# Performance work log

Measured on AMD Instinct MI355X. Metric: run time of the kernel, lower is better.

Reference implementation:

```python
import jax, jax.numpy as jnp
import numpy as np

# Hyperparameters from module __init__
U_TH = 1.0      # firing threshold
BETA = 0.5      # membrane decay
BATCH_SIZE = 128
DELTA = 0.05    # ZO smoothing radius


def setup_inputs() -> dict:
    key = jax.random.key(0)
    k1, k2 = jax.random.split(key)
    T, B, F = 32, BATCH_SIZE, 8192
    inputs = jax.random.normal(k1, (T * B, F), dtype=jnp.float32)
    # 'sample once' Gaussian ZO tangents, same shape as inputs
    random_tangents = jax.random.normal(k2, (T * B, F), dtype=jnp.float32)
    return {"inputs": inputs, "random_tangents": random_tangents}


def reference(inputs, random_tangents):
    """Leaky integrate-and-fire over time with LocalZO (single-sample)
    surrogate gradient. inputs: [T*B, F] with T = leading//BATCH_SIZE."""
    orig_shape = inputs.shape
    T = inputs.shape[0] // BATCH_SIZE
    x = inputs.reshape(T, BATCH_SIZE, *inputs.shape[1:])
    z = random_tangents.reshape(T, BATCH_SIZE, *inputs.shape[1:])

    def step(u, xt_zt):
        xt, zt = xt_zt
        u = BETA * u + xt                      # membrane update
        v = u - U_TH                           # distance to threshold
        # LocalZO single-sample surrogate: |z|/(2*delta) * 1(|v| < delta*|z|)
        surr = jax.lax.stop_gradient(
            (jnp.abs(zt) / (2.0 * DELTA))
            * (jnp.abs(v) < DELTA * jnp.abs(zt)).astype(xt.dtype)
        )
        h = (v > 0).astype(xt.dtype)           # hard spike
        # straight-through: forward = h, d spike / d v = surr
        spike = jax.lax.stop_gradient(h - surr * v) + surr * v
        u = u - spike * U_TH                   # soft reset (subtract threshold)
        return u, spike

    u0 = jnp.zeros_like(x[0])
    _, spikes = jax.lax.scan(step, u0, (x, z))
    return spikes.reshape(orig_shape)
```

## Files before the change

kernel.cpp:

```cpp
#include <hip/hip_runtime.h>


constexpr int BATCH = 128;
constexpr int FDIM  = 8192;
constexpr int STEP  = BATCH * FDIM;
constexpr int VEC   = 2;

typedef float v2f __attribute__((ext_vector_type(2)));

__global__ __launch_bounds__(256) void lif_zo_kernel(
    const float* __restrict__ x,
    const float* __restrict__ z,
    float* __restrict__ out,
    int T)
{
#pragma clang fp contract(off)
    const int tid = blockIdx.x * blockDim.x + threadIdx.x;
    long idx = (long)tid * VEC;

    float u[VEC];
#pragma unroll
    for (int c = 0; c < VEC; ++c) u[c] = 0.0f;

    v2f xt = *reinterpret_cast<const v2f*>(x + idx);
    v2f zt = *reinterpret_cast<const v2f*>(z + idx);

    for (int t = 0; t < T; ++t) {
        const long nidx = idx + STEP;
        const long pidx = (t + 1 < T) ? nidx : idx;
        const v2f xn = *reinterpret_cast<const v2f*>(x + pidx);
        const v2f zn = *reinterpret_cast<const v2f*>(z + pidx);

        v2f ss;
#pragma unroll
        for (int c = 0; c < VEC; ++c) {
            float uu = 0.5f * u[c];
            uu = uu + xt[c];
            float v = uu - 1.0f;
            float az   = fabsf(zt[c]);
            float thr  = 0.05f * az;
            float ind  = (fabsf(v) < thr) ? 1.0f : 0.0f;
            float surr = (az / 0.1f) * ind;
            float h = (v > 0.0f) ? 1.0f : 0.0f;
            float a     = surr * v;
            float spike = (h - a) + a;
            u[c] = uu - spike * 1.0f;
            ss[c] = spike;
        }
        __builtin_nontemporal_store(ss, reinterpret_cast<v2f*>(out + idx));

        xt = xn; zt = zn;
        idx = nidx;
    }
}

extern "C" void kernel_launch(void* const* d_in, const int* in_sizes, int n_in,
                              void* d_out, int out_size, void* d_ws, size_t ws_size,
                              hipStream_t stream)
{
    const float* x = (const float*)d_in[0];
    const float* z = (const float*)d_in[1];
    float* out = (float*)d_out;

    const int total = in_sizes[0];
    const int T = total / STEP;

    const int nthreads = STEP / VEC;
    const int block = 256;
    const int grid = nthreads / block;

    lif_zo_kernel<<<grid, block, 0, stream>>>(x, z, out, T);
}
```

Baseline: 326.1 us.

## Deepen time-step prefetch to four steps ahead with rotating register buffers

Replaces the one-step-ahead load double buffer with a four-deep rotating register prefetch, so each thread keeps four time steps of x and z loads in flight. The loop is unrolled by four and the output store switches from nontemporal to a regular store. It also adds an occupancy hint to launch bounds. The aim is more memory-level parallelism on this bandwidth-bound scan, at the cost of more registers. The loop assumes T is a multiple of four.

```diff
diff --git a/kernel.cpp b/kernel.cpp
--- a/kernel.cpp
+++ b/kernel.cpp
@@ -5,10 +5,11 @@
 constexpr int FDIM  = 8192;
 constexpr int STEP  = BATCH * FDIM;
 constexpr int VEC   = 2;
+constexpr int PF    = 4;
 
 typedef float v2f __attribute__((ext_vector_type(2)));
 
-__global__ __launch_bounds__(256) void lif_zo_kernel(
+__global__ __launch_bounds__(256, 8) void lif_zo_kernel(
     const float* __restrict__ x,
     const float* __restrict__ z,
     float* __restrict__ out,
@@ -16,41 +17,74 @@
 {
 #pragma clang fp contract(off)
     const int tid = blockIdx.x * blockDim.x + threadIdx.x;
-    long idx = (long)tid * VEC;
+    const long base = (long)tid * VEC;
 
-    float u[VEC];
-#pragma unroll
-    for (int c = 0; c < VEC; ++c) u[c] = 0.0f;
+    float u0 = 0.0f, u1 = 0.0f;
 
-    v2f xt = *reinterpret_cast<const v2f*>(x + idx);
-    v2f zt = *reinterpret_cast<const v2f*>(z + idx);
+    v2f xb0 = *reinterpret_cast<const v2f*>(x + base + 0L * STEP);
+    v2f zb0 = *reinterpret_cast<const v2f*>(z + base + 0L * STEP);
+    v2f xb1 = *reinterpret_cast<const v2f*>(x + base + 1L * STEP);
+    v2f zb1 = *reinterpret_cast<const v2f*>(z + base + 1L * STEP);
+    v2f xb2 = *reinterpret_cast<const v2f*>(x + base + 2L * STEP);
+    v2f zb2 = *reinterpret_cast<const v2f*>(z + base + 2L * STEP);
+    v2f xb3 = *reinterpret_cast<const v2f*>(x + base + 3L * STEP);
+    v2f zb3 = *reinterpret_cast<const v2f*>(z + base + 3L * STEP);
 
-    for (int t = 0; t < T; ++t) {
-        const long nidx = idx + STEP;
-        const long pidx = (t + 1 < T) ? nidx : idx;
-        const v2f xn = *reinterpret_cast<const v2f*>(x + pidx);
-        const v2f zn = *reinterpret_cast<const v2f*>(z + pidx);
+    auto lif = [&](const v2f xt, const v2f zt) -> v2f {
+        v2f ss;
+        float uu, v, az, thr, ind, surr, h, a, spike;
+        uu = 0.5f * u0; uu = uu + xt[0];
+        v  = uu - 1.0f;
+        az = fabsf(zt[0]); thr = 0.05f * az;
+        ind = (fabsf(v) < thr) ? 1.0f : 0.0f;
+        surr = (az / 0.1f) * ind;
+        h = (v > 0.0f) ? 1.0f : 0.0f;
+        a = surr * v; spike = (h - a) + a;
+        u0 = uu - spike * 1.0f; ss[0] = spike;
+        uu = 0.5f * u1; uu = uu + xt[1];
+        v  = uu - 1.0f;
+        az = fabsf(zt[1]); thr = 0.05f * az;
+        ind = (fabsf(v) < thr) ? 1.0f : 0.0f;
+        surr = (az / 0.1f) * ind;
+        h = (v > 0.0f) ? 1.0f : 0.0f;
+        a = surr * v; spike = (h - a) + a;
+        u1 = uu - spike * 1.0f; ss[1] = spike;
+        return ss;
+    };
 
-        v2f ss;
-#pragma unroll
-        for (int c = 0; c < VEC; ++c) {
-            float uu = 0.5f * u[c];
-            uu = uu + xt[c];
-            float v = uu - 1.0f;
-            float az   = fabsf(zt[c]);
-            float thr  = 0.05f * az;
-            float ind  = (fabsf(v) < thr) ? 1.0f : 0.0f;
-            float surr = (az / 0.1f) * ind;
-            float h = (v > 0.0f) ? 1.0f : 0.0f;
-            float a     = surr * v;
-            float spike = (h - a) + a;
-            u[c] = uu - spike * 1.0f;
-            ss[c] = spike;
+    for (int t = 0; t < T; t += PF) {
+        {
+            const long pt  = (t + 0 + PF < T) ? (long)(t + 0 + PF) : (long)(T - 1);
+            const v2f xn = *reinterpret_cast<const v2f*>(x + base + pt * STEP);
+            const v2f zn = *reinterpret_cast<const v2f*>(z + base + pt * STEP);
+            v2f ss = lif(xb0, zb0);
+            *reinterpret_cast<v2f*>(out + base + (long)(t + 0) * STEP) = ss;
+            xb0 = xn; zb0 = zn;
         }
-        __builtin_nontemporal_store(ss, reinterpret_cast<v2f*>(out + idx));
-
-        xt = xn; zt = zn;
-        idx = nidx;
+        {
+            const long pt  = (t + 1 + PF < T) ? (long)(t + 1 + PF) : (long)(T - 1);
+            const v2f xn = *reinterpret_cast<const v2f*>(x + base + pt * STEP);
+            const v2f zn = *reinterpret_cast<const v2f*>(z + base + pt * STEP);
+            v2f ss = lif(xb1, zb1);
+            *reinterpret_cast<v2f*>(out + base + (long)(t + 1) * STEP) = ss;
+            xb1 = xn; zb1 = zn;
+        }
+        {
+            const long pt  = (t + 2 + PF < T) ? (long)(t + 2 + PF) : (long)(T - 1);
+            const v2f xn = *reinterpret_cast<const v2f*>(x + base + pt * STEP);
+            const v2f zn = *reinterpret_cast<const v2f*>(z + base + pt * STEP);
+            v2f ss = lif(xb2, zb2);
+            *reinterpret_cast<v2f*>(out + base + (long)(t + 2) * STEP) = ss;
+            xb2 = xn; zb2 = zn;
+        }
+        {
+            const long pt  = (t + 3 + PF < T) ? (long)(t + 3 + PF) : (long)(T - 1);
+            const v2f xn = *reinterpret_cast<const v2f*>(x + base + pt * STEP);
+            const v2f zn = *reinterpret_cast<const v2f*>(z + base + pt * STEP);
+            v2f ss = lif(xb3, zb3);
+            *reinterpret_cast<v2f*>(out + base + (long)(t + 3) * STEP) = ss;
+            xb3 = xn; zb3 = zn;
+        }
     }
 }
 
```

Measured after the change: 313.3 us. -3.9%, faster.
